# Performance work log

Hardware: AMD Instinct MI355X
Metric: run time of the kernel (lower is better)

## Reference

```python
import jax, jax.numpy as jnp
import numpy as np

B, L, D = 2, 2048, 2048
H, HKV, HD = 32, 8, 64
G = H // HKV  # GQA group size


def _rope(t, cos, sin):
    # t: [B, h, L, HD]; cos/sin: [L, HD//2]; pairs are consecutive (view_as_complex)
    tr, ti = t[..., 0::2], t[..., 1::2]
    out_r = tr * cos - ti * sin
    out_i = tr * sin + ti * cos
    return jnp.stack([out_r, out_i], axis=-1).reshape(t.shape)


def setup_inputs() -> dict:
    key = jax.random.key(0)
    ks = jax.random.split(key, 5)
    x = jax.random.normal(ks[0], (B, L, D), dtype=jnp.float32)
    wq = jax.random.normal(ks[1], (D, H * HD), dtype=jnp.float32) * 0.02
    wk = jax.random.normal(ks[2], (D, HKV * HD), dtype=jnp.float32) * 0.02
    wv = jax.random.normal(ks[3], (D, HKV * HD), dtype=jnp.float32) * 0.02
    wo = jax.random.normal(ks[4], (D, D), dtype=jnp.float32) * 0.02
    # RoPE freqs: theta_i = 10000^(-2i/HD), angle[p, i] = p * theta_i
    inv_freq = 1.0 / (10000.0 ** (jnp.arange(0, HD, 2, dtype=jnp.float32) / HD))
    angles = jnp.arange(L, dtype=jnp.float32)[:, None] * inv_freq[None, :]  # [L, HD//2]
    freqs_cos = jnp.cos(angles)
    freqs_sin = jnp.sin(angles)
    # additive causal mask [L, L]
    mask = jnp.where(jnp.tril(jnp.ones((L, L), dtype=bool)), 0.0, -1e9).astype(jnp.float32)
    return {"x": x, "wq": wq, "wk": wk, "wv": wv, "wo": wo,
            "freqs_cos": freqs_cos, "freqs_sin": freqs_sin, "mask": mask}


def reference(x, wq, wk, wv, wo, freqs_cos, freqs_sin, mask):
    b, l, _ = x.shape
    q = (x @ wq).reshape(b, l, H, HD).transpose(0, 2, 1, 3)      # [B, H, L, HD]
    k = (x @ wk).reshape(b, l, HKV, HD).transpose(0, 2, 1, 3)    # [B, HKV, L, HD]
    v = (x @ wv).reshape(b, l, HKV, HD).transpose(0, 2, 1, 3)
    q = _rope(q, freqs_cos, freqs_sin)
    k = _rope(k, freqs_cos, freqs_sin)
    # native GQA broadcast instead of repeat_kv copy (same math)
    qg = q.reshape(b, HKV, G, l, HD)
    scores = jnp.einsum("bhgqd,bhkd->bhgqk", qg, k) / jnp.sqrt(jnp.float32(HD))
    scores = scores + mask  # [B, HKV, G, L, L]
    probs = jax.nn.softmax(scores.astype(jnp.float32), axis=-1).astype(v.dtype)
    out = jnp.einsum("bhgqk,bhkd->bhgqd", probs, v)              # [B, HKV, G, L, HD]
    out = out.reshape(b, H, l, HD).transpose(0, 2, 1, 3).reshape(b, l, H * HD)
    return out @ wo
```

## Files before the change

kernel.cpp:

```cpp
#include <hip/hip_runtime.h>
#include <hip/hip_bf16.h>

#define B_   2
#define L_   2048
#define D_   2048
#define H_   32
#define HKV_ 8
#define HD_  64
#define G_   4
#define M_   4096
#define NF_  3072

typedef __attribute__((ext_vector_type(8))) short bf16x8;
typedef __attribute__((ext_vector_type(4))) float f32x4;

static __device__ __forceinline__ unsigned short f2bf(float f) {
  unsigned int u = __float_as_uint(f);
  unsigned int r = (u + 0x7FFFu + ((u >> 16) & 1u)) >> 16;
  return (unsigned short)r;
}
static __device__ __forceinline__ unsigned short f2bf_hw(float f) {
  __hip_bfloat16 h = __float2bfloat16(f);
  return *(unsigned short*)&h;
}

#define GLD16(g, l) __builtin_amdgcn_global_load_lds(                      \
    (const __attribute__((address_space(1))) void*)(g),                    \
    (__attribute__((address_space(3))) void*)(l), 16, 0, 0)

__global__ void cast_bf16_kernel(const float* __restrict__ in,
                                 unsigned short* __restrict__ out, int n4) {
  int i = blockIdx.x * blockDim.x + threadIdx.x;
  if (i >= n4) return;
  float4 v = ((const float4*)in)[i];
  uint2 r;
  r.x = (unsigned int)f2bf(v.x) | ((unsigned int)f2bf(v.y) << 16);
  r.y = (unsigned int)f2bf(v.z) | ((unsigned int)f2bf(v.w) << 16);
  ((uint2*)out)[i] = r;
}

__global__ void transpose_cast_kernel(const float* __restrict__ src,
                                      unsigned short* __restrict__ dst,
                                      int K, int N) {
  __shared__ float tile[32][33];
  int k0 = blockIdx.y * 32, n0 = blockIdx.x * 32;
  int tx = threadIdx.x, ty = threadIdx.y;
#pragma unroll
  for (int r = 0; r < 4; ++r)
    tile[ty * 4 + r][tx] = src[(size_t)(k0 + ty * 4 + r) * N + n0 + tx];
  __syncthreads();
#pragma unroll
  for (int r = 0; r < 4; ++r)
    dst[(size_t)(n0 + ty * 4 + r) * K + k0 + tx] = f2bf(tile[tx][ty * 4 + r]);
}

__global__ void transpose_cast_qkv_kernel(const float* __restrict__ wq,
                                          const float* __restrict__ wk,
                                          const float* __restrict__ wv,
                                          unsigned short* __restrict__ dst) {
  __shared__ float tile[32][33];
  int n0 = blockIdx.x * 32, k0 = blockIdx.y * 32;
  const float* src;
  int ns, N;
  if (n0 < 2048)      { src = wq; ns = n0;        N = 2048; }
  else if (n0 < 2560) { src = wk; ns = n0 - 2048; N = 512; }
  else                { src = wv; ns = n0 - 2560; N = 512; }
  int tx = threadIdx.x, ty = threadIdx.y;
#pragma unroll
  for (int r = 0; r < 4; ++r)
    tile[ty * 4 + r][tx] = src[(size_t)(k0 + ty * 4 + r) * N + ns + tx];
  __syncthreads();
#pragma unroll
  for (int r = 0; r < 4; ++r)
    dst[(size_t)(n0 + ty * 4 + r) * 2048 + k0 + tx] = f2bf(tile[tx][ty * 4 + r]);
}

__global__ __launch_bounds__(512)
void gemm256x128_kernel(const unsigned short* __restrict__ A,
                        const unsigned short* __restrict__ Bt,
                        float* __restrict__ C, int M, int N, int K) {
  __shared__ unsigned short Al[2][256 * 32];
  __shared__ unsigned short Bl[2][128 * 32];
  const int tid = threadIdx.x;
  const int w = tid >> 6, l = tid & 63;
  const int wave_m = w >> 1, wave_n = w & 1;
  const int row0 = blockIdx.y * 256, col0 = blockIdx.x * 128;
  const int fr = l & 15, fk = (l >> 4) * 8;
  const int srow = l >> 2, scol = (l & 3) * 8;
  const int nk = K >> 5;

  f32x4 acc[4][4];
#pragma unroll
  for (int m = 0; m < 4; ++m)
#pragma unroll
    for (int n = 0; n < 4; ++n) acc[m][n] = (f32x4){0.f, 0.f, 0.f, 0.f};

#define GSTAGE(buf_, kt_) do {                                               \
    GLD16(A + (size_t)(row0 + w * 16 + srow) * K + (kt_) * 32 + scol,        \
          &Al[buf_][w * 512]);                                               \
    GLD16(A + (size_t)(row0 + 128 + w * 16 + srow) * K + (kt_) * 32 + scol,  \
          &Al[buf_][(8 + w) * 512]);                                         \
    GLD16(Bt + (size_t)(col0 + w * 16 + srow) * K + (kt_) * 32 + scol,       \
          &Bl[buf_][w * 512]);                                               \
  } while (0)

  GSTAGE(0, 0);

  for (int kt = 0; kt < nk; ++kt) {
    const int buf = kt & 1;
    if (kt + 1 < nk) {
      GSTAGE(buf ^ 1, kt + 1);
      asm volatile("s_waitcnt vmcnt(3)" ::: "memory");
    } else {
      asm volatile("s_waitcnt vmcnt(0)" ::: "memory");
    }
    __builtin_amdgcn_s_barrier();

    bf16x8 af[4], bfr[4];
#pragma unroll
    for (int m = 0; m < 4; ++m)
      af[m] = *(const bf16x8*)&Al[buf][(wave_m * 64 + m * 16 + fr) * 32 + fk];
#pragma unroll
    for (int n = 0; n < 4; ++n)
      bfr[n] = *(const bf16x8*)&Bl[buf][(wave_n * 64 + n * 16 + fr) * 32 + fk];
    __builtin_amdgcn_s_setprio(1);
#pragma unroll
    for (int m = 0; m < 4; ++m)
#pragma unroll
      for (int n = 0; n < 4; ++n)
        acc[m][n] = __builtin_amdgcn_mfma_f32_16x16x32_bf16(af[m], bfr[n], acc[m][n], 0, 0, 0);
    __builtin_amdgcn_s_setprio(0);
    __builtin_amdgcn_s_barrier();
  }
#undef GSTAGE

  const int fq = l >> 4;
#pragma unroll
  for (int m = 0; m < 4; ++m)
#pragma unroll
    for (int n = 0; n < 4; ++n)
#pragma unroll
      for (int j = 0; j < 4; ++j) {
        int r = row0 + wave_m * 64 + m * 16 + fq * 4 + j;
        int c = col0 + wave_n * 64 + n * 16 + fr;
        C[(size_t)r * N + c] = acc[m][n][j];
      }
}

__global__ void rope_kernel(const float* __restrict__ src,
                            const float* __restrict__ cosf,
                            const float* __restrict__ sinf,
                            unsigned short* __restrict__ dst, int nh, int col_off,
                            float scale, int total) {
  int idx = blockIdx.x * blockDim.x + threadIdx.x;
  if (idx >= total) return;
  int g = idx & 7;
  int h = (idx >> 3) & (nh - 1);
  int row = idx / (nh << 3);
  int lpos = row & (L_ - 1);
  int b = row >> 11;
  const float* s = src + (size_t)row * NF_ + col_off + h * 64 + g * 8;
  float4 v0 = *(const float4*)s;
  float4 v1 = *(const float4*)(s + 4);
  float4 c4 = *(const float4*)(cosf + lpos * 32 + g * 4);
  float4 s4 = *(const float4*)(sinf + lpos * 32 + g * 4);
  float o0 = (v0.x * c4.x - v0.y * s4.x) * scale;
  float o1 = (v0.x * s4.x + v0.y * c4.x) * scale;
  float o2 = (v0.z * c4.y - v0.w * s4.y) * scale;
  float o3 = (v0.z * s4.y + v0.w * c4.y) * scale;
  float o4 = (v1.x * c4.z - v1.y * s4.z) * scale;
  float o5 = (v1.x * s4.z + v1.y * c4.z) * scale;
  float o6 = (v1.z * c4.w - v1.w * s4.w) * scale;
  float o7 = (v1.z * s4.w + v1.w * c4.w) * scale;
  uint4 r;
  r.x = (unsigned int)f2bf(o0) | ((unsigned int)f2bf(o1) << 16);
  r.y = (unsigned int)f2bf(o2) | ((unsigned int)f2bf(o3) << 16);
  r.z = (unsigned int)f2bf(o4) | ((unsigned int)f2bf(o5) << 16);
  r.w = (unsigned int)f2bf(o6) | ((unsigned int)f2bf(o7) << 16);
  *(uint4*)&dst[(((size_t)(b * nh + h)) * L_ + lpos) * 64 + g * 8] = r;
}

__global__ void cast_vT_kernel(const float* __restrict__ v,
                               unsigned short* __restrict__ vT) {
  __shared__ float tile[32][33];
  int l0 = blockIdx.x * 32, d0 = blockIdx.y * 32;
  int z = blockIdx.z;
  int b = z >> 3, hkv = z & 7;
  int tx = threadIdx.x, ty = threadIdx.y;
  const float* src = v + (size_t)(b * L_) * NF_ + 2560 + hkv * 64;
#pragma unroll
  for (int r = 0; r < 4; ++r)
    tile[ty * 4 + r][tx] = src[(size_t)(l0 + ty * 4 + r) * NF_ + d0 + tx];
  __syncthreads();
  unsigned short* dst = vT + ((size_t)z * 64) * L_;
#pragma unroll
  for (int r = 0; r < 4; ++r)
    dst[(size_t)(d0 + ty * 4 + r) * L_ + l0 + tx] = f2bf(tile[tx][ty * 4 + r]);
}

__global__ __launch_bounds__(256)
void attn_kernel(const unsigned short* __restrict__ Q,
                 const unsigned short* __restrict__ Kt,
                 const unsigned short* __restrict__ Vt,
                 unsigned short* __restrict__ O) {
  __shared__ unsigned short Kl[2][64 * 64];
  __shared__ unsigned short Vl[2][64 * 64];
  __shared__ unsigned short Pl[64 * 64];
  const int tid = threadIdx.x, w = tid >> 6, l = tid & 63;
  const int lin = blockIdx.y * 8 + blockIdx.x;
  const int work = ((lin & 7) << 6) + (lin >> 3);
  const int bh = work >> 3, pr = work & 7;
  const int b = bh >> 5, h = bh & 31;
  const int hkv = h >> 2;
  const int fr = l & 15, hi = l >> 4;
  const int frx = fr & 7;

  const int srow = l >> 3;
  const int scole = ((l & 7) ^ srow) * 8;

  const unsigned short* kbase = Kt + ((size_t)(b * HKV_ + hkv)) * L_ * 64;
  const unsigned short* vbase = Vt + ((size_t)(b * HKV_ + hkv)) * 64 * L_;

#define ASTAGE(kv0_, buf_) do {                                              \
    _Pragma("unroll")                                                        \
    for (int u_ = 0; u_ < 2; ++u_) {                                         \
      const int c_ = w * 2 + u_;                                             \
      const int rr_ = c_ * 8 + srow;                                         \
      GLD16(kbase + ((size_t)((kv0_) + rr_)) * 64 + scole,                   \
            &Kl[buf_][c_ * 512]);                                            \
      GLD16(vbase + ((size_t)rr_) * L_ + (kv0_) + scole,                     \
            &Vl[buf_][c_ * 512]);                                            \
    }                                                                        \
  } while (0)

  for (int half = 0; half < 2; ++half) {
    const int by = half ? (15 - pr) : pr;
    const int q0 = by * 128;

    bf16x8 qf[2][2];
#pragma unroll
    for (int s = 0; s < 2; ++s) {
      const unsigned short* qb =
          Q + (((size_t)bh) * L_ + q0 + s * 64 + w * 16 + fr) * 64 + hi * 8;
      qf[s][0] = *(const bf16x8*)(qb);
      qf[s][1] = *(const bf16x8*)(qb + 32);
    }

    float m_i[2][4], l_p[2][4];
    f32x4 oacc[2][4];
#pragma unroll
    for (int s = 0; s < 2; ++s)
#pragma unroll
      for (int j = 0; j < 4; ++j) { m_i[s][j] = -1e30f; l_p[s][j] = 0.f; }
#pragma unroll
    for (int s = 0; s < 2; ++s)
#pragma unroll
      for (int nf = 0; nf < 4; ++nf) oacc[s][nf] = (f32x4){0.f, 0.f, 0.f, 0.f};

    const int nt = 2 * by + 2;

    ASTAGE(0, 0);

    for (int t = 0; t < nt; ++t) {
      const int buf = t & 1;
      if (t + 1 < nt) {
        ASTAGE((t + 1) * 64, buf ^ 1);
        asm volatile("s_waitcnt vmcnt(4)" ::: "memory");
      } else {
        asm volatile("s_waitcnt vmcnt(0)" ::: "memory");
      }
      __builtin_amdgcn_s_barrier();

      const int kv0 = t * 64;
#pragma unroll
      for (int s = 0; s < 2; ++s) {
        const int dlim = 2 * by + s;
        if (t > dlim) continue;

        f32x4 sacc[4];
#pragma unroll
        for (int nf = 0; nf < 4; ++nf) sacc[nf] = (f32x4){0.f, 0.f, 0.f, 0.f};
        __builtin_amdgcn_s_setprio(1);
#pragma unroll
        for (int ks = 0; ks < 2; ++ks) {
#pragma unroll
          for (int nf = 0; nf < 4; ++nf) {
            bf16x8 kfrag = *(const bf16x8*)
                &Kl[buf][(nf * 16 + fr) * 64 + (((ks * 4 + hi) ^ frx) * 8)];
            sacc[nf] = __builtin_amdgcn_mfma_f32_16x16x32_bf16(qf[s][ks], kfrag, sacc[nf], 0, 0, 0);
          }
        }
        __builtin_amdgcn_s_setprio(0);

        if (t == dlim) {
          const int rbase = q0 + s * 64 + w * 16 + hi * 4;
#pragma unroll
          for (int nf = 0; nf < 4; ++nf)
#pragma unroll
            for (int j = 0; j < 4; ++j)
              if (kv0 + nf * 16 + fr > rbase + j) sacc[nf][j] = -1e30f;
        }

        float rowmax[4];
#pragma unroll
        for (int j = 0; j < 4; ++j) {
          float mx = fmaxf(fmaxf(sacc[0][j], sacc[1][j]),
                           fmaxf(sacc[2][j], sacc[3][j]));
          mx = fmaxf(mx, __shfl_xor(mx, 1));
          mx = fmaxf(mx, __shfl_xor(mx, 2));
          mx = fmaxf(mx, __shfl_xor(mx, 4));
          mx = fmaxf(mx, __shfl_xor(mx, 8));
          rowmax[j] = mx;
        }

        float g = rowmax[0] - m_i[s][0];
        g = fmaxf(g, rowmax[1] - m_i[s][1]);
        g = fmaxf(g, rowmax[2] - m_i[s][2]);
        g = fmaxf(g, rowmax[3] - m_i[s][3]);
        if (!__all(g <= 8.f)) {
#pragma unroll
          for (int j = 0; j < 4; ++j) {
            float mnew = fmaxf(m_i[s][j], rowmax[j]);
            float cr = exp2f(m_i[s][j] - mnew);
            m_i[s][j] = mnew;
            l_p[s][j] *= cr;
#pragma unroll
            for (int nf = 0; nf < 4; ++nf) oacc[s][nf][j] *= cr;
          }
        }

#pragma unroll
        for (int j = 0; j < 4; ++j) {
          const int prow = w * 16 + hi * 4 + j;
#pragma unroll
          for (int nf = 0; nf < 4; ++nf) {
            float pv = exp2f(sacc[nf][j] - m_i[s][j]);
            l_p[s][j] += pv;
            Pl[prow * 64 + (((nf * 2 + (fr >> 3)) ^ (prow & 7)) * 8) + frx] =
                f2bf_hw(pv);
          }
        }

        __builtin_amdgcn_s_setprio(1);
#pragma unroll
        for (int ks = 0; ks < 2; ++ks) {
          bf16x8 pa = *(const bf16x8*)
              &Pl[(w * 16 + fr) * 64 + (((ks * 4 + hi) ^ frx) * 8)];
#pragma unroll
          for (int nf = 0; nf < 4; ++nf) {
            bf16x8 vfrag = *(const bf16x8*)
                &Vl[buf][(nf * 16 + fr) * 64 + (((ks * 4 + hi) ^ frx) * 8)];
            oacc[s][nf] = __builtin_amdgcn_mfma_f32_16x16x32_bf16(pa, vfrag, oacc[s][nf], 0, 0, 0);
          }
        }
        __builtin_amdgcn_s_setprio(0);
      }
      __builtin_amdgcn_s_barrier();
    }

#pragma unroll
    for (int s = 0; s < 2; ++s)
#pragma unroll
      for (int j = 0; j < 4; ++j) {
        float lsum = l_p[s][j];
        lsum += __shfl_xor(lsum, 1);
        lsum += __shfl_xor(lsum, 2);
        lsum += __shfl_xor(lsum, 4);
        lsum += __shfl_xor(lsum, 8);
        float inv = 1.0f / lsum;
#pragma unroll
        for (int nf = 0; nf < 4; ++nf) {
          int qrow = q0 + s * 64 + w * 16 + hi * 4 + j;
          int d = nf * 16 + fr;
          O[((size_t)(b * L_ + qrow)) * 2048 + h * 64 + d] =
              f2bf_hw(oacc[s][nf][j] * inv);
        }
      }
  }
#undef ASTAGE
}

extern "C" void kernel_launch(void* const* d_in, const int* in_sizes, int n_in,
                              void* d_out, int out_size, void* d_ws, size_t ws_size,
                              hipStream_t stream) {
  (void)in_sizes; (void)n_in; (void)out_size; (void)ws_size;
  const float* x  = (const float*)d_in[0];
  const float* wq = (const float*)d_in[1];
  const float* wk = (const float*)d_in[2];
  const float* wv = (const float*)d_in[3];
  const float* wo = (const float*)d_in[4];
  const float* fc = (const float*)d_in[5];
  const float* fs = (const float*)d_in[6];
  float* out = (float*)d_out;

  char* ws = (char*)d_ws;
  unsigned short* x_b  = (unsigned short*)(ws + 0);
  unsigned short* wT   = (unsigned short*)(ws + 16777216);
  unsigned short* woT  = (unsigned short*)(ws + 29360128);
  float* qkv_f         = (float*)(ws + 37748736);
  unsigned short* at_b = (unsigned short*)(ws + 37748736);
  unsigned short* q_b  = (unsigned short*)(ws + 88080384);
  unsigned short* k_b  = (unsigned short*)(ws + 104857600);
  unsigned short* vT_b = (unsigned short*)(ws + 109051904);

  const float qscale = 0.125f * 1.4426950408889634f;

  dim3 tb(32, 8);
  cast_bf16_kernel<<<8192, 256, 0, stream>>>(x, x_b, M_ * D_ / 4);
  transpose_cast_qkv_kernel<<<dim3(96, 64), tb, 0, stream>>>(wq, wk, wv, wT);
  transpose_cast_kernel<<<dim3(64, 64), tb, 0, stream>>>(wo, woT, 2048, 2048);

  gemm256x128_kernel<<<dim3(NF_ / 128, M_ / 256), 512, 0, stream>>>(
      x_b, wT, qkv_f, M_, NF_, 2048);

  rope_kernel<<<4096, 256, 0, stream>>>(qkv_f, fc, fs, q_b, 32, 0, qscale, M_ * 32 * 8);
  rope_kernel<<<1024, 256, 0, stream>>>(qkv_f, fc, fs, k_b, 8, 2048, 1.0f, M_ * 8 * 8);
  cast_vT_kernel<<<dim3(64, 2, 16), tb, 0, stream>>>(qkv_f, vT_b);

  attn_kernel<<<dim3(8, 64), 256, 0, stream>>>(q_b, k_b, vT_b, at_b);

  gemm256x128_kernel<<<dim3(2048 / 128, M_ / 256), 512, 0, stream>>>(
      at_b, woT, out, M_, 2048, 2048);
}
```

Before: 387.4 us.

## Store QKV projection in bf16 and single-buffer attention K/V tiles

The QKV GEMM now writes bf16 instead of fp32, so rope and the V transpose read half as many bytes and the fp32 intermediate round trip goes away. This adds one extra rounding of Q/K before RoPE is applied. Separately, the attention kernel drops its double-buffered K/V LDS prefetch and uses a synchronous load followed by __syncthreads on each tile. That cuts LDS use but exposes global load latency, since loads no longer overlap with compute.

```diff
diff --git a/kernel.cpp b/kernel.cpp
--- a/kernel.cpp
+++ b/kernel.cpp
@@ -22,6 +22,9 @@
 static __device__ __forceinline__ unsigned short f2bf_hw(float f) {
   __hip_bfloat16 h = __float2bfloat16(f);
   return *(unsigned short*)&h;
+}
+static __device__ __forceinline__ float bf2f(unsigned short u) {
+  return __uint_as_float(((unsigned int)u) << 16);
 }
 
 #define GLD16(g, l) __builtin_amdgcn_global_load_lds(                      \
@@ -75,10 +78,11 @@
     dst[(size_t)(n0 + ty * 4 + r) * 2048 + k0 + tx] = f2bf(tile[tx][ty * 4 + r]);
 }
 
+template <typename OUT_T>
 __global__ __launch_bounds__(512)
 void gemm256x128_kernel(const unsigned short* __restrict__ A,
                         const unsigned short* __restrict__ Bt,
-                        float* __restrict__ C, int M, int N, int K) {
+                        OUT_T* __restrict__ C, int M, int N, int K) {
   __shared__ unsigned short Al[2][256 * 32];
   __shared__ unsigned short Bl[2][128 * 32];
   const int tid = threadIdx.x;
@@ -143,11 +147,14 @@
       for (int j = 0; j < 4; ++j) {
         int r = row0 + wave_m * 64 + m * 16 + fq * 4 + j;
         int c = col0 + wave_n * 64 + n * 16 + fr;
-        C[(size_t)r * N + c] = acc[m][n][j];
+        if constexpr (sizeof(OUT_T) == 2)
+          C[(size_t)r * N + c] = f2bf_hw(acc[m][n][j]);
+        else
+          C[(size_t)r * N + c] = acc[m][n][j];
       }
 }
 
-__global__ void rope_kernel(const float* __restrict__ src,
+__global__ void rope_kernel(const unsigned short* __restrict__ src,
                             const float* __restrict__ cosf,
                             const float* __restrict__ sinf,
                             unsigned short* __restrict__ dst, int nh, int col_off,
@@ -159,19 +166,21 @@
   int row = idx / (nh << 3);
   int lpos = row & (L_ - 1);
   int b = row >> 11;
-  const float* s = src + (size_t)row * NF_ + col_off + h * 64 + g * 8;
-  float4 v0 = *(const float4*)s;
-  float4 v1 = *(const float4*)(s + 4);
+  bf16x8 v = *(const bf16x8*)(src + (size_t)row * NF_ + col_off + h * 64 + g * 8);
   float4 c4 = *(const float4*)(cosf + lpos * 32 + g * 4);
   float4 s4 = *(const float4*)(sinf + lpos * 32 + g * 4);
-  float o0 = (v0.x * c4.x - v0.y * s4.x) * scale;
-  float o1 = (v0.x * s4.x + v0.y * c4.x) * scale;
-  float o2 = (v0.z * c4.y - v0.w * s4.y) * scale;
-  float o3 = (v0.z * s4.y + v0.w * c4.y) * scale;
-  float o4 = (v1.x * c4.z - v1.y * s4.z) * scale;
-  float o5 = (v1.x * s4.z + v1.y * c4.z) * scale;
-  float o6 = (v1.z * c4.w - v1.w * s4.w) * scale;
-  float o7 = (v1.z * s4.w + v1.w * c4.w) * scale;
+  float e0 = bf2f((unsigned short)v[0]), e1 = bf2f((unsigned short)v[1]);
+  float e2 = bf2f((unsigned short)v[2]), e3 = bf2f((unsigned short)v[3]);
+  float e4 = bf2f((unsigned short)v[4]), e5 = bf2f((unsigned short)v[5]);
+  float e6 = bf2f((unsigned short)v[6]), e7 = bf2f((unsigned short)v[7]);
+  float o0 = (e0 * c4.x - e1 * s4.x) * scale;
+  float o1 = (e0 * s4.x + e1 * c4.x) * scale;
+  float o2 = (e2 * c4.y - e3 * s4.y) * scale;
+  float o3 = (e2 * s4.y + e3 * c4.y) * scale;
+  float o4 = (e4 * c4.z - e5 * s4.z) * scale;
+  float o5 = (e4 * s4.z + e5 * c4.z) * scale;
+  float o6 = (e6 * c4.w - e7 * s4.w) * scale;
+  float o7 = (e6 * s4.w + e7 * c4.w) * scale;
   uint4 r;
   r.x = (unsigned int)f2bf(o0) | ((unsigned int)f2bf(o1) << 16);
   r.y = (unsigned int)f2bf(o2) | ((unsigned int)f2bf(o3) << 16);
@@ -180,14 +189,14 @@
   *(uint4*)&dst[(((size_t)(b * nh + h)) * L_ + lpos) * 64 + g * 8] = r;
 }
 
-__global__ void cast_vT_kernel(const float* __restrict__ v,
+__global__ void cast_vT_kernel(const unsigned short* __restrict__ v,
                                unsigned short* __restrict__ vT) {
-  __shared__ float tile[32][33];
+  __shared__ unsigned short tile[32][33];
   int l0 = blockIdx.x * 32, d0 = blockIdx.y * 32;
   int z = blockIdx.z;
   int b = z >> 3, hkv = z & 7;
   int tx = threadIdx.x, ty = threadIdx.y;
-  const float* src = v + (size_t)(b * L_) * NF_ + 2560 + hkv * 64;
+  const unsigned short* src = v + (size_t)(b * L_) * NF_ + 2560 + hkv * 64;
 #pragma unroll
   for (int r = 0; r < 4; ++r)
     tile[ty * 4 + r][tx] = src[(size_t)(l0 + ty * 4 + r) * NF_ + d0 + tx];
@@ -195,7 +204,7 @@
   unsigned short* dst = vT + ((size_t)z * 64) * L_;
 #pragma unroll
   for (int r = 0; r < 4; ++r)
-    dst[(size_t)(d0 + ty * 4 + r) * L_ + l0 + tx] = f2bf(tile[tx][ty * 4 + r]);
+    dst[(size_t)(d0 + ty * 4 + r) * L_ + l0 + tx] = tile[tx][ty * 4 + r];
 }
 
 __global__ __launch_bounds__(256)
@@ -203,13 +212,13 @@
                  const unsigned short* __restrict__ Kt,
                  const unsigned short* __restrict__ Vt,
                  unsigned short* __restrict__ O) {
-  __shared__ unsigned short Kl[2][64 * 64];
-  __shared__ unsigned short Vl[2][64 * 64];
+  __shared__ unsigned short Kl[64 * 64];
+  __shared__ unsigned short Vl[64 * 64];
   __shared__ unsigned short Pl[64 * 64];
   const int tid = threadIdx.x, w = tid >> 6, l = tid & 63;
   const int lin = blockIdx.y * 8 + blockIdx.x;
   const int work = ((lin & 7) << 6) + (lin >> 3);
-  const int bh = work >> 3, pr = work & 7;
+  const int bh = work >> 3, pair = work & 7;
   const int b = bh >> 5, h = bh & 31;
   const int hkv = h >> 2;
   const int fr = l & 15, hi = l >> 4;
@@ -221,20 +230,8 @@
   const unsigned short* kbase = Kt + ((size_t)(b * HKV_ + hkv)) * L_ * 64;
   const unsigned short* vbase = Vt + ((size_t)(b * HKV_ + hkv)) * 64 * L_;
 
-#define ASTAGE(kv0_, buf_) do {                                              \
-    _Pragma("unroll")                                                        \
-    for (int u_ = 0; u_ < 2; ++u_) {                                         \
-      const int c_ = w * 2 + u_;                                             \
-      const int rr_ = c_ * 8 + srow;                                         \
-      GLD16(kbase + ((size_t)((kv0_) + rr_)) * 64 + scole,                   \
-            &Kl[buf_][c_ * 512]);                                            \
-      GLD16(vbase + ((size_t)rr_) * L_ + (kv0_) + scole,                     \
-            &Vl[buf_][c_ * 512]);                                            \
-    }                                                                        \
-  } while (0)
-
   for (int half = 0; half < 2; ++half) {
-    const int by = half ? (15 - pr) : pr;
+    const int by = half ? (15 - pair) : pair;
     const int q0 = by * 128;
 
     bf16x8 qf[2][2];
@@ -259,19 +256,17 @@
 
     const int nt = 2 * by + 2;
 
-    ASTAGE(0, 0);
-
     for (int t = 0; t < nt; ++t) {
-      const int buf = t & 1;
-      if (t + 1 < nt) {
-        ASTAGE((t + 1) * 64, buf ^ 1);
-        asm volatile("s_waitcnt vmcnt(4)" ::: "memory");
-      } else {
-        asm volatile("s_waitcnt vmcnt(0)" ::: "memory");
+      const int kv0 = t * 64;
+#pragma unroll
+      for (int u = 0; u < 2; ++u) {
+        const int c = w * 2 + u;
+        const int rr = c * 8 + srow;
+        GLD16(kbase + ((size_t)(kv0 + rr)) * 64 + scole, &Kl[c * 512]);
+        GLD16(vbase + ((size_t)rr) * L_ + kv0 + scole, &Vl[c * 512]);
       }
-      __builtin_amdgcn_s_barrier();
-
-      const int kv0 = t * 64;
+      __syncthreads();
+
 #pragma unroll
       for (int s = 0; s < 2; ++s) {
         const int dlim = 2 * by + s;
@@ -286,7 +281,7 @@
 #pragma unroll
           for (int nf = 0; nf < 4; ++nf) {
             bf16x8 kfrag = *(const bf16x8*)
-                &Kl[buf][(nf * 16 + fr) * 64 + (((ks * 4 + hi) ^ frx) * 8)];
+                &Kl[(nf * 16 + fr) * 64 + (((ks * 4 + hi) ^ frx) * 8)];
             sacc[nf] = __builtin_amdgcn_mfma_f32_16x16x32_bf16(qf[s][ks], kfrag, sacc[nf], 0, 0, 0);
           }
         }
@@ -349,13 +344,13 @@
 #pragma unroll
           for (int nf = 0; nf < 4; ++nf) {
             bf16x8 vfrag = *(const bf16x8*)
-                &Vl[buf][(nf * 16 + fr) * 64 + (((ks * 4 + hi) ^ frx) * 8)];
+                &Vl[(nf * 16 + fr) * 64 + (((ks * 4 + hi) ^ frx) * 8)];
             oacc[s][nf] = __builtin_amdgcn_mfma_f32_16x16x32_bf16(pa, vfrag, oacc[s][nf], 0, 0, 0);
           }
         }
         __builtin_amdgcn_s_setprio(0);
       }
-      __builtin_amdgcn_s_barrier();
+      __syncthreads();
     }
 
 #pragma unroll
@@ -377,7 +372,6 @@
         }
       }
   }
-#undef ASTAGE
 }
 
 extern "C" void kernel_launch(void* const* d_in, const int* in_sizes, int n_in,
@@ -394,14 +388,14 @@
   float* out = (float*)d_out;
 
   char* ws = (char*)d_ws;
-  unsigned short* x_b  = (unsigned short*)(ws + 0);
-  unsigned short* wT   = (unsigned short*)(ws + 16777216);
-  unsigned short* woT  = (unsigned short*)(ws + 29360128);
-  float* qkv_f         = (float*)(ws + 37748736);
-  unsigned short* at_b = (unsigned short*)(ws + 37748736);
-  unsigned short* q_b  = (unsigned short*)(ws + 88080384);
-  unsigned short* k_b  = (unsigned short*)(ws + 104857600);
-  unsigned short* vT_b = (unsigned short*)(ws + 109051904);
+  unsigned short* x_b   = (unsigned short*)(ws + 0);
+  unsigned short* wT    = (unsigned short*)(ws + 16777216);
+  unsigned short* woT   = (unsigned short*)(ws + 29360128);
+  unsigned short* qkv_b = (unsigned short*)(ws + 37748736);
+  unsigned short* at_b  = (unsigned short*)(ws + 62914560);
+  unsigned short* q_b   = (unsigned short*)(ws + 88080384);
+  unsigned short* k_b   = (unsigned short*)(ws + 104857600);
+  unsigned short* vT_b  = (unsigned short*)(ws + 109051904);
 
   const float qscale = 0.125f * 1.4426950408889634f;
 
@@ -410,15 +404,15 @@
   transpose_cast_qkv_kernel<<<dim3(96, 64), tb, 0, stream>>>(wq, wk, wv, wT);
   transpose_cast_kernel<<<dim3(64, 64), tb, 0, stream>>>(wo, woT, 2048, 2048);
 
-  gemm256x128_kernel<<<dim3(NF_ / 128, M_ / 256), 512, 0, stream>>>(
-      x_b, wT, qkv_f, M_, NF_, 2048);
-
-  rope_kernel<<<4096, 256, 0, stream>>>(qkv_f, fc, fs, q_b, 32, 0, qscale, M_ * 32 * 8);
-  rope_kernel<<<1024, 256, 0, stream>>>(qkv_f, fc, fs, k_b, 8, 2048, 1.0f, M_ * 8 * 8);
-  cast_vT_kernel<<<dim3(64, 2, 16), tb, 0, stream>>>(qkv_f, vT_b);
+  gemm256x128_kernel<unsigned short><<<dim3(NF_ / 128, M_ / 256), 512, 0, stream>>>(
+      x_b, wT, qkv_b, M_, NF_, 2048);
+
+  rope_kernel<<<4096, 256, 0, stream>>>(qkv_b, fc, fs, q_b, 32, 0, qscale, M_ * 32 * 8);
+  rope_kernel<<<1024, 256, 0, stream>>>(qkv_b, fc, fs, k_b, 8, 2048, 1.0f, M_ * 8 * 8);
+  cast_vT_kernel<<<dim3(64, 2, 16), tb, 0, stream>>>(qkv_b, vT_b);
 
   attn_kernel<<<dim3(8, 64), 256, 0, stream>>>(q_b, k_b, vT_b, at_b);
 
-  gemm256x128_kernel<<<dim3(2048 / 128, M_ / 256), 512, 0, stream>>>(
+  gemm256x128_kernel<float><<<dim3(2048 / 128, M_ / 256), 512, 0, stream>>>(
       at_b, woT, out, M_, 2048, 2048);
 }
```

Measured after the change: 379.4 us. 1.02x faster.
